# Performance work log

Measured on AMD Instinct MI355X. Metric: run time of the kernel, lower is better.

The kernel has to match this reference:

```python
import jax, jax.numpy as jnp
import numpy as np

N = 50000   # nodes
E = 800000  # edges (avg degree 16)
D = 128     # input = hidden = embedding dim
K1 = 25000  # ceil(0.5 * N)
K2 = 12500  # ceil(0.5 * K1)
LABELS = 5
BN_EPS = 1e-5


def _sage(x, src, dst, W, b, normalize):
    # old-PyG SAGEConv: remove self loops, add self loop, mean aggregate, linear, L2-normalize
    n = x.shape[0]
    dst_e = jnp.where(src == dst, n, dst)  # drop self loops; dummy edges (src=dst=n) also land in segment n
    s = jax.ops.segment_sum(x[src], dst_e, num_segments=n + 1)[:n]          # [n, d]
    deg = jax.ops.segment_sum(jnp.ones(src.shape, x.dtype), dst_e, num_segments=n + 1)[:n]
    agg = (s + x) / (deg + 1.0)[:, None]  # mean over neighbors + self
    out = agg @ W + b
    if normalize:
        out = out / jnp.maximum(jnp.linalg.norm(out, axis=-1, keepdims=True), 1e-12)
    return out


def _bn(x, g, b):
    # training-mode BatchNorm1d over nodes (biased variance, like torch)
    m = x.mean(axis=0)
    v = jnp.var(x, axis=0)
    return (x - m) / jnp.sqrt(v + BN_EPS) * g + b


def _sag_pool(x, src, dst, wp, bp, k):
    # SAGPooling: score = tanh(SAGEConv(x)->1), global top_k (single graph), filter_adj via dummy remap
    n = x.shape[0]
    score = jnp.tanh(_sage(x, src, dst, wp[:, None], bp, normalize=False)[:, 0])  # [n]
    score_k, perm = jax.lax.top_k(score, k)
    x2 = x[perm] * score_k[:, None]
    rank = jnp.full((n + 1,), -1, jnp.int32).at[perm].set(jnp.arange(k, dtype=jnp.int32))
    rs, rd = rank[src], rank[dst]
    valid = (rs >= 0) & (rd >= 0)
    src2 = jnp.where(valid, rs, k)  # invalid edges -> dummy node k
    dst2 = jnp.where(valid, rd, k)
    return x2, src2, dst2


def _forward(x, edge_index, Wc, bc, gamma, beta, Wpool, bpool, W1, b1, W2, b2):
    src, dst = edge_index[0], edge_index[1]
    # source bug replicated: stage 3 layer 2 uses bn_3_1's params
    bn_idx = [[0, 1, 2], [3, 4, 5], [6, 6, 8]]
    ks = [K1, K2]
    outs = []
    for s in range(3):
        for i in range(3):
            li = 3 * s + i
            x = jax.nn.relu(_sage(x, src, dst, Wc[li], bc[li], True))
            bi = bn_idx[s][i]
            x = _bn(x, gamma[bi], beta[bi])
        outs.append(jnp.max(x, axis=0))  # scatter_max with a single graph
        if s < 2:
            x, src, dst = _sag_pool(x, src, dst, Wpool[s], bpool[s], ks[s])
    h = jnp.concatenate(outs)[None, :]          # [1, 3*D]
    h = jax.nn.relu(h @ W1 + b1)
    return h @ W2 + b2                           # [1, LABELS]


def setup_inputs() -> dict:
    key = jax.random.key(0)
    ks = jax.random.split(key, 8)
    x = jax.random.normal(ks[0], (N, D), dtype=jnp.float32)
    edge_index = jax.random.randint(ks[1], (2, E), 0, N, dtype=jnp.int32)
    Wc = jax.random.normal(ks[2], (9, D, D), dtype=jnp.float32) / np.sqrt(D)
    bc = jnp.zeros((9, D), jnp.float32)
    gamma = jnp.ones((9, D), jnp.float32)
    beta = jnp.zeros((9, D), jnp.float32)
    Wpool = jax.random.normal(ks[3], (2, D), dtype=jnp.float32) / np.sqrt(D)
    bpool = jnp.zeros((2,), jnp.float32)
    W1 = jax.random.normal(ks[4], (3 * D, 50), dtype=jnp.float32) / np.sqrt(3 * D)
    b1 = jnp.zeros((50,), jnp.float32)
    W2 = jax.random.normal(ks[5], (50, LABELS), dtype=jnp.float32) / np.sqrt(50)
    b2 = jnp.zeros((LABELS,), jnp.float32)
    return {"x": x, "edge_index": edge_index, "Wc": Wc, "bc": bc, "gamma": gamma,
            "beta": beta, "Wpool": Wpool, "bpool": bpool,
            "W1": W1, "b1": b1, "W2": W2, "b2": b2}


def reference(x, edge_index, Wc, bc, gamma, beta, Wpool, bpool, W1, b1, W2, b2):
    return _forward(x, edge_index, Wc, bc, gamma, beta, Wpool, bpool, W1, b1, W2, b2)
```

## Files before the change

kernel.cpp:

```cpp
#include <hip/hip_runtime.h>

constexpr int FD   = 128;
constexpr int NMAX = 50000;
constexpr int EDG  = 800000;

static __device__ __forceinline__ unsigned enc(float f){
  unsigned u = __float_as_uint(f);
  return (u & 0x80000000u) ? ~u : (u | 0x80000000u);
}
static __device__ __forceinline__ float dec(unsigned e){
  unsigned u = (e & 0x80000000u) ? (e ^ 0x80000000u) : ~e;
  return __uint_as_float(u);
}

__global__ void k_count(const int* __restrict__ src, const int* __restrict__ dst,
                        int* __restrict__ deg, int E){
  int e = blockIdx.x*256 + threadIdx.x;
  if (e >= E) return;
  int s = src[e], d = dst[e];
  if (s != d) atomicAdd(&deg[d], 1);
}

__global__ void k_remap_count(const int* __restrict__ sIn, const int* __restrict__ dIn,
                              int* __restrict__ sOut, int* __restrict__ dOut,
                              const int* __restrict__ rank, int kNew,
                              int* __restrict__ deg, int E){
  int e = blockIdx.x*256 + threadIdx.x;
  if (e >= E) return;
  int s = sIn[e], d = dIn[e];
  int rs = rank[s], rd = rank[d];
  bool ok = (rs >= 0) && (rd >= 0);
  int os = ok ? rs : kNew, od = ok ? rd : kNew;
  sOut[e] = os; dOut[e] = od;
  if (os != od) atomicAdd(&deg[od], 1);
}

__global__ __launch_bounds__(256) void k_offsets(const int* __restrict__ deg,
    int* __restrict__ start, int* __restrict__ cur, int* __restrict__ total, int n){
  __shared__ int wsum[4];
  __shared__ int sbase;
  int tid = threadIdx.x, lane = tid & 63, wid = tid >> 6;
  int v = blockIdx.x*256 + tid;
  int x = (v < n) ? deg[v] : 0;
  int val = x;
  #pragma unroll
  for (int o = 1; o < 64; o <<= 1){ int t = __shfl_up(val, o); if (lane >= o) val += t; }
  if (lane == 63) wsum[wid] = val;
  __syncthreads();
  if (tid == 0){
    int t0 = wsum[0], t1 = wsum[1], t2 = wsum[2], t3 = wsum[3];
    sbase = atomicAdd(total, t0+t1+t2+t3);
    wsum[0] = 0; wsum[1] = t0; wsum[2] = t0+t1; wsum[3] = t0+t1+t2;
  }
  __syncthreads();
  int excl = (val - x) + wsum[wid] + sbase;
  if (v < n){ start[v] = excl; cur[v] = excl; }
}

__global__ void k_fill(const int* __restrict__ src, const int* __restrict__ dst,
                       int* __restrict__ cur, int* __restrict__ csr, int E){
  int e = blockIdx.x*256 + threadIdx.x;
  if (e >= E) return;
  int s = src[e], d = dst[e];
  if (s != d){ int pos = atomicAdd(&cur[d], 1); csr[pos] = s; }
}

__global__ __launch_bounds__(256) void k_agg(const float* __restrict__ X,
    const int* __restrict__ start, const int* __restrict__ degb,
    const int* __restrict__ csr,
    float* __restrict__ AGG, int n,
    const float* __restrict__ st, const float* __restrict__ g,
    const float* __restrict__ bt, float invn){
  int tid = threadIdx.x;
  int v = blockIdx.x*4 + (tid >> 6);
  if (v >= n) return;
  int lane = tid & 63;
  int c = lane * 2;
  float ax = 1.f, ay = 1.f, bx = 0.f, by = 0.f;
  if (st){
    float ma = st[c]*invn, mb = st[c+1]*invn;
    float va = st[FD+c]*invn - ma*ma, vb = st[FD+c+1]*invn - mb*mb;
    ax = g[c]*rsqrtf(va + 1e-5f);  ay = g[c+1]*rsqrtf(vb + 1e-5f);
    bx = bt[c] - ma*ax;            by = bt[c+1] - mb*ay;
  }
  int b = start[v];
  int deg = degb[v];
  float2 s = *(const float2*)(X + (size_t)v*FD + c);
  int j = 0;
  while (j < deg){
    int cnt = deg - j; if (cnt > 64) cnt = 64;
    int myu = (j + lane < deg) ? csr[b + j + lane] : 0;
    int t = 0;
    for (; t + 8 <= cnt; t += 8){
      int u0 = __shfl(myu, t),   u1 = __shfl(myu, t+1);
      int u2 = __shfl(myu, t+2), u3 = __shfl(myu, t+3);
      int u4 = __shfl(myu, t+4), u5 = __shfl(myu, t+5);
      int u6 = __shfl(myu, t+6), u7 = __shfl(myu, t+7);
      float2 t0 = *(const float2*)(X + (size_t)u0*FD + c);
      float2 t1 = *(const float2*)(X + (size_t)u1*FD + c);
      float2 t2 = *(const float2*)(X + (size_t)u2*FD + c);
      float2 t3 = *(const float2*)(X + (size_t)u3*FD + c);
      float2 t4 = *(const float2*)(X + (size_t)u4*FD + c);
      float2 t5 = *(const float2*)(X + (size_t)u5*FD + c);
      float2 t6 = *(const float2*)(X + (size_t)u6*FD + c);
      float2 t7 = *(const float2*)(X + (size_t)u7*FD + c);
      s.x += ((t0.x + t1.x) + (t2.x + t3.x)) + ((t4.x + t5.x) + (t6.x + t7.x));
      s.y += ((t0.y + t1.y) + (t2.y + t3.y)) + ((t4.y + t5.y) + (t6.y + t7.y));
    }
    for (; t + 4 <= cnt; t += 4){
      int u0 = __shfl(myu, t),   u1 = __shfl(myu, t+1);
      int u2 = __shfl(myu, t+2), u3 = __shfl(myu, t+3);
      float2 t0 = *(const float2*)(X + (size_t)u0*FD + c);
      float2 t1 = *(const float2*)(X + (size_t)u1*FD + c);
      float2 t2 = *(const float2*)(X + (size_t)u2*FD + c);
      float2 t3 = *(const float2*)(X + (size_t)u3*FD + c);
      s.x += (t0.x + t1.x) + (t2.x + t3.x);
      s.y += (t0.y + t1.y) + (t2.y + t3.y);
    }
    for (; t < cnt; t++){
      int u = __shfl(myu, t);
      float2 tt = *(const float2*)(X + (size_t)u*FD + c);
      s.x += tt.x; s.y += tt.y;
    }
    j += cnt;
  }
  float inv = 1.f / (float)(deg + 1);
  float2 o;
  o.x = s.x*inv*ax + bx;
  o.y = s.y*inv*ay + by;
  *(float2*)(AGG + (size_t)v*FD + c) = o;
}

__global__ __launch_bounds__(256,2) void k_gemm(const float* __restrict__ A,
    const float* __restrict__ W, const float* __restrict__ bias,
    float* __restrict__ Y, float* __restrict__ stats, int n,
    unsigned* __restrict__ cmx, unsigned* __restrict__ cmn){
  __shared__ float sW[FD*FD];
  __shared__ float ss[4][FD];
  __shared__ float sq_[4][FD];
  __shared__ float smx[4][FD];
  __shared__ float smn[4][FD];
  int tid = threadIdx.x;
  {
    const float4* Wg = (const float4*)W; float4* Ws = (float4*)sW;
    for (int i = tid; i < FD*FD/4; i += 256) Ws[i] = Wg[i];
  }
  __syncthreads();
  int tc = tid & 15;
  int tr = tid >> 4;
  int rbase = blockIdx.x*FD + tr*8;
  float acc[8][8];
  #pragma unroll
  for (int i = 0; i < 8; i++)
    #pragma unroll
    for (int j = 0; j < 8; j++) acc[i][j] = 0.f;

  for (int k4 = 0; k4 < FD; k4 += 4){
    float4 a[8];
    #pragma unroll
    for (int i = 0; i < 8; i++){
      int r = rbase + i; if (r >= n) r = n - 1;
      a[i] = *(const float4*)(A + (size_t)r*FD + k4);
    }
    #pragma unroll
    for (int kk = 0; kk < 4; kk++){
      const float* wr = &sW[(k4+kk)*FD + tc*8];
      float4 w0 = *(const float4*)wr, w1 = *(const float4*)(wr+4);
      #pragma unroll
      for (int i = 0; i < 8; i++){
        float av = (kk==0) ? a[i].x : (kk==1) ? a[i].y : (kk==2) ? a[i].z : a[i].w;
        acc[i][0] += av*w0.x; acc[i][1] += av*w0.y; acc[i][2] += av*w0.z; acc[i][3] += av*w0.w;
        acc[i][4] += av*w1.x; acc[i][5] += av*w1.y; acc[i][6] += av*w1.z; acc[i][7] += av*w1.w;
      }
    }
  }
  float bx[8];
  {
    const float* bp = bias + tc*8;
    #pragma unroll
    for (int j = 0; j < 8; j++) bx[j] = bp[j];
  }
  float cs[8], cq[8], mxv[8], mnv[8];
  #pragma unroll
  for (int j = 0; j < 8; j++){ cs[j]=0.f; cq[j]=0.f; mxv[j]=-3.4e38f; mnv[j]=3.4e38f; }
  #pragma unroll
  for (int i = 0; i < 8; i++){
    int r = rbase + i;
    bool valid = (r < n);
    float y[8]; float sq = 0.f;
    #pragma unroll
    for (int j = 0; j < 8; j++){ y[j] = acc[i][j] + bx[j]; sq += y[j]*y[j]; }
    sq += __shfl_xor(sq,1); sq += __shfl_xor(sq,2); sq += __shfl_xor(sq,4); sq += __shfl_xor(sq,8);
    float nrm = sqrtf(sq);
    float sc = 1.f / fmaxf(nrm, 1e-12f);
    #pragma unroll
    for (int j = 0; j < 8; j++){ y[j] *= sc; y[j] = fmaxf(y[j], 0.f); }
    if (valid){
      float* yo = Y + (size_t)r*FD + tc*8;
      *(float4*)yo     = make_float4(y[0],y[1],y[2],y[3]);
      *(float4*)(yo+4) = make_float4(y[4],y[5],y[6],y[7]);
      #pragma unroll
      for (int j = 0; j < 8; j++){
        cs[j] += y[j]; cq[j] += y[j]*y[j];
        mxv[j] = fmaxf(mxv[j], y[j]); mnv[j] = fminf(mnv[j], y[j]);
      }
    }
  }
  #pragma unroll
  for (int j = 0; j < 8; j++){
    cs[j] += __shfl_xor(cs[j],16); cs[j] += __shfl_xor(cs[j],32);
    cq[j] += __shfl_xor(cq[j],16); cq[j] += __shfl_xor(cq[j],32);
    mxv[j] = fmaxf(mxv[j], __shfl_xor(mxv[j],16)); mxv[j] = fmaxf(mxv[j], __shfl_xor(mxv[j],32));
    mnv[j] = fminf(mnv[j], __shfl_xor(mnv[j],16)); mnv[j] = fminf(mnv[j], __shfl_xor(mnv[j],32));
  }
  int wv = tid >> 6, lane = tid & 63;
  if (lane < 16){
    #pragma unroll
    for (int j = 0; j < 8; j++){
      ss[wv][tc*8+j] = cs[j]; sq_[wv][tc*8+j] = cq[j];
      smx[wv][tc*8+j] = mxv[j]; smn[wv][tc*8+j] = mnv[j];
    }
  }
  __syncthreads();
  if (tid < FD){
    float s_ = ss[0][tid]+ss[1][tid]+ss[2][tid]+ss[3][tid];
    float q_ = sq_[0][tid]+sq_[1][tid]+sq_[2][tid]+sq_[3][tid];
    atomicAdd(&stats[tid], s_);
    atomicAdd(&stats[FD+tid], q_);
    if (cmx){
      float mx = fmaxf(fmaxf(smx[0][tid],smx[1][tid]), fmaxf(smx[2][tid],smx[3][tid]));
      float mn = fminf(fminf(smn[0][tid],smn[1][tid]), fminf(smn[2][tid],smn[3][tid]));
      atomicMax(&cmx[tid], enc(mx));
      atomicMin(&cmn[tid], enc(mn));
    }
  }
}

__global__ __launch_bounds__(256) void k_dotp(const float* __restrict__ X,
    const float* __restrict__ wp,
    const float* __restrict__ st, const float* __restrict__ g,
    const float* __restrict__ bt, float invn,
    float* __restrict__ p, int n){
  int tid = threadIdx.x;
  int v = blockIdx.x*4 + (tid >> 6), lane = tid & 63;
  if (v >= n) return;
  int c = lane * 2;
  float ma = st[c]*invn, mb = st[c+1]*invn;
  float va = st[FD+c]*invn - ma*ma, vb = st[FD+c+1]*invn - mb*mb;
  float ax = g[c]*rsqrtf(va + 1e-5f), ay = g[c+1]*rsqrtf(vb + 1e-5f);
  float bx = bt[c] - ma*ax,           by = bt[c+1] - mb*ay;
  float2 x = *(const float2*)(X + (size_t)v*FD + c);
  float2 w = *(const float2*)(wp + c);
  float s = (ax*x.x + bx)*w.x + (ay*x.y + by)*w.y;
  s += __shfl_xor(s,1); s += __shfl_xor(s,2); s += __shfl_xor(s,4);
  s += __shfl_xor(s,8); s += __shfl_xor(s,16); s += __shfl_xor(s,32);
  if (lane == 0) p[v] = s;
}

__global__ void k_score(const float* __restrict__ p, const int* __restrict__ start,
    const int* __restrict__ degb, const int* __restrict__ csr,
    const float* __restrict__ bpool, int pi,
    float* __restrict__ score, unsigned* __restrict__ hist, int n){
  int v = blockIdx.x*256 + threadIdx.x;
  if (v >= n) return;
  int b = start[v], deg = degb[v];
  float s = p[v];
  for (int j = 0; j < deg; j++) s += p[csr[b+j]];
  float sc = tanhf(s / (float)(deg + 1) + bpool[pi]);
  score[v] = sc;
  atomicAdd(&hist[enc(sc) >> 16], 1u);
}

__global__ void k_hist_lo(const float* __restrict__ score, int n,
                          const unsigned* __restrict__ state, unsigned* __restrict__ hist){
  int v = blockIdx.x*256 + threadIdx.x;
  if (v >= n) return;
  unsigned key = enc(score[v]);
  if ((key >> 16) == state[5]) atomicAdd(&hist[key & 0xFFFFu], 1u);
}

__global__ __launch_bounds__(1024) void k_pick(const unsigned* __restrict__ hist,
                                               unsigned* __restrict__ state, int k, int pass){
  __shared__ unsigned wsum[16];
  int tid = threadIdx.x;
  unsigned want = (pass == 0) ? (unsigned)k : state[4];
  unsigned prevAbove = (pass == 0) ? 0u : state[1];
  int chunk = 1023 - tid;
  const unsigned* hbase = hist + chunk*64;
  unsigned csum = 0;
  #pragma unroll
  for (int j = 0; j < 64; j++) csum += hbase[j];
  unsigned val = csum;
  int lane = tid & 63, wid = tid >> 6;
  #pragma unroll
  for (int o = 1; o < 64; o <<= 1){ unsigned t = __shfl_up(val, o); if (lane >= o) val += t; }
  if (lane == 63) wsum[wid] = val;
  __syncthreads();
  if (tid < 16){
    unsigned v2 = wsum[tid];
    #pragma unroll
    for (int o = 1; o < 16; o <<= 1){ unsigned t = __shfl_up(v2, o); if (tid >= o) v2 += t; }
    wsum[tid] = v2;
  }
  __syncthreads();
  unsigned incl = val + ((wid > 0) ? wsum[wid-1] : 0u);
  unsigned excl = incl - csum;
  if (excl < want && incl >= want){
    unsigned cum = excl, above = 0; int bsel = 0;
    for (int j = 63; j >= 0; j--){
      unsigned cc = hbase[j];
      if (cum + cc >= want){ bsel = j; above = cum; break; }
      cum += cc;
    }
    unsigned bucket = (unsigned)(chunk*64 + bsel);
    if (pass == 0){
      state[5] = bucket;
      state[1] = prevAbove + above;
      state[4] = want - above;
    } else {
      unsigned T = (state[5] << 16) | bucket;
      unsigned totAbove = prevAbove + above;
      state[0] = T; state[1] = totAbove; state[2] = 0u; state[3] = totAbove;
    }
  }
}

__global__ void k_compact(const float* __restrict__ score, unsigned* __restrict__ state,
    int* __restrict__ rank, int* __restrict__ sel, int n, int k){
  int v = blockIdx.x*256 + threadIdx.x;
  if (v > n) return;
  if (v == n){ rank[n] = -1; return; }
  unsigned T = state[0];
  unsigned key = enc(score[v]);
  int slot = -1;
  if (key > T) slot = (int)atomicAdd(&state[2], 1u);
  else if (key == T){ unsigned t = atomicAdd(&state[3], 1u); if (t < (unsigned)k) slot = (int)t; }
  rank[v] = slot;
  if (slot >= 0) sel[slot] = v;
}

__global__ __launch_bounds__(256) void k_gather(const float* __restrict__ X,
    const int* __restrict__ sel, const float* __restrict__ score,
    const float* __restrict__ st, const float* __restrict__ g,
    const float* __restrict__ bt, float invn,
    float* __restrict__ XO, int k){
  int j = blockIdx.x*4 + (threadIdx.x >> 6), lane = threadIdx.x & 63;
  if (j >= k) return;
  int c = lane * 2;
  float ma = st[c]*invn, mb = st[c+1]*invn;
  float va = st[FD+c]*invn - ma*ma, vb = st[FD+c+1]*invn - mb*mb;
  float ax = g[c]*rsqrtf(va + 1e-5f), ay = g[c+1]*rsqrtf(vb + 1e-5f);
  float bx = bt[c] - ma*ax,           by = bt[c+1] - mb*ay;
  int u = sel[j];
  float sc = score[u];
  float2 t = *(const float2*)(X + (size_t)u*FD + c);
  t.x = (ax*t.x + bx)*sc; t.y = (ay*t.y + by)*sc;
  *(float2*)(XO + (size_t)j*FD + c) = t;
}

__global__ void k_final(const unsigned* __restrict__ cmx, const unsigned* __restrict__ cmn,
    const float* __restrict__ stats, const float* __restrict__ gamma,
    const float* __restrict__ beta,
    const float* __restrict__ W1, const float* __restrict__ b1,
    const float* __restrict__ W2, const float* __restrict__ b2,
    float* __restrict__ out){
  __shared__ float h[384];
  __shared__ float h1[50];
  int tid = threadIdx.x;
  if (tid < 384){
    int s = tid >> 7, c = tid & 127;
    const int liR[3] = {2,5,8};
    const float nsf[3] = {50000.f, 25000.f, 12500.f};
    int li = liR[s];
    const float* st = stats + (size_t)li*256;
    float invn = 1.f / nsf[s];
    float m = st[c]*invn, vv = st[FD+c]*invn - m*m;
    float a = gamma[(size_t)li*FD+c]*rsqrtf(vv + 1e-5f);
    float bb = beta[(size_t)li*FD+c] - m*a;
    float mx = dec(cmx[tid]), mn = dec(cmn[tid]);
    h[tid] = (a >= 0.f) ? (a*mx + bb) : (a*mn + bb);
  }
  __syncthreads();
  if (tid < 50){
    float acc = b1[tid];
    for (int i = 0; i < 384; i++) acc += h[i]*W1[i*50 + tid];
    h1[tid] = fmaxf(acc, 0.f);
  }
  __syncthreads();
  if (tid < 5){
    float acc = b2[tid];
    for (int i = 0; i < 50; i++) acc += h1[i]*W2[i*5 + tid];
    out[tid] = acc;
  }
}

extern "C" void kernel_launch(void* const* d_in, const int* in_sizes, int n_in,
                              void* d_out, int out_size, void* d_ws, size_t ws_size,
                              hipStream_t stream){
  (void)in_sizes; (void)n_in; (void)out_size; (void)ws_size;
  const float* x_in  = (const float*)d_in[0];
  const int*   ei    = (const int*)d_in[1];
  const float* Wc    = (const float*)d_in[2];
  const float* bc    = (const float*)d_in[3];
  const float* gamma = (const float*)d_in[4];
  const float* beta  = (const float*)d_in[5];
  const float* Wpool = (const float*)d_in[6];
  const float* bpool = (const float*)d_in[7];
  const float* W1    = (const float*)d_in[8];
  const float* b1    = (const float*)d_in[9];
  const float* W2    = (const float*)d_in[10];
  const float* b2    = (const float*)d_in[11];
  float* dout = (float*)d_out;

  char* base = (char*)d_ws; size_t o_ = 0;
  auto alloc = [&](size_t bytes)->void*{
    void* p = base + o_; o_ = (o_ + bytes + 255) & ~(size_t)255; return p;
  };
  float* B0   = (float*)alloc((size_t)NMAX*FD*4);
  float* B1   = (float*)alloc((size_t)NMAX*FD*4);
  int* eSrc   = (int*)alloc((size_t)EDG*4);
  int* eDst   = (int*)alloc((size_t)EDG*4);
  int* degb   = (int*)alloc((size_t)(NMAX+1)*4);
  int* startv = (int*)alloc((size_t)NMAX*4);
  int* cur    = (int*)alloc((size_t)NMAX*4);
  int* csr    = (int*)alloc((size_t)EDG*4);
  float* pbuf = (float*)alloc((size_t)NMAX*4);
  float* sbuf = (float*)alloc((size_t)NMAX*4);
  int* sel    = (int*)alloc((size_t)25000*4);
  int* rank   = (int*)alloc((size_t)(NMAX+1)*4);
  float* stats= (float*)alloc(9*256*4);
  unsigned* cmx = (unsigned*)alloc(384*4);
  unsigned* cmn = (unsigned*)alloc(384*4);
  unsigned* state= (unsigned*)alloc(64);
  unsigned* hist = (unsigned*)alloc(2*65536*4);

  const int ns[3]  = {50000, 25000, 12500};
  const int bnIdx[9] = {0,1,2,3,4,5,6,6,8};
  const int EB = (EDG + 255)/256;

  hipMemsetAsync(stats, 0, 9*256*4, stream);
  hipMemsetAsync(cmx, 0x00, 384*4, stream);
  hipMemsetAsync(cmn, 0xFF, 384*4, stream);

  const int* cs = ei;
  const int* cd = ei + EDG;

  for (int s = 0; s < 3; s++){
    int n = ns[s];
    float fin = 1.f/(float)n;
    float* X = (s == 1) ? B1 : B0;
    float* A = (s == 1) ? B0 : B1;

    hipMemsetAsync(degb, 0, (size_t)(n+1)*4, stream);
    if (s == 0){
      k_count<<<dim3(EB), dim3(256), 0, stream>>>(cs, cd, degb, EDG);
    } else {
      k_remap_count<<<dim3(EB), dim3(256), 0, stream>>>(cs, cd, eSrc, eDst, rank, n, degb, EDG);
      cs = eSrc; cd = eDst;
    }
    k_offsets<<<dim3((n+255)/256), dim3(256), 0, stream>>>(degb, startv, cur, degb + n, n);
    k_fill<<<dim3(EB), dim3(256), 0, stream>>>(cs, cd, cur, csr, EDG);

    for (int i = 0; i < 3; i++){
      int li = s*3 + i;
      const float* xr = (s == 0 && i == 0) ? x_in : (const float*)X;
      const float* stPrev = (i == 0) ? (const float*)nullptr : stats + (size_t)(li-1)*256;
      int gb = (i == 0) ? 0 : bnIdx[li-1];
      bool rd = (i == 2);
      k_agg<<<dim3((n+3)/4), dim3(256), 0, stream>>>(xr, startv, degb, csr, A, n,
                                                     stPrev, gamma + (size_t)gb*FD, beta + (size_t)gb*FD, fin);
      k_gemm<<<dim3((n+FD-1)/FD), dim3(256), 0, stream>>>(A, Wc + (size_t)li*FD*FD, bc + li*FD, X,
                                                          stats + (size_t)li*256, n,
                                                          rd ? (cmx + s*FD) : (unsigned*)nullptr,
                                                          rd ? (cmn + s*FD) : (unsigned*)nullptr);
    }

    if (s < 2){
      int k = (s == 0) ? 25000 : 12500;
      int li2 = s*3 + 2;
      const float* st2 = stats + (size_t)li2*256;
      const float* g2 = gamma + (size_t)bnIdx[li2]*FD;
      const float* bt2 = beta + (size_t)bnIdx[li2]*FD;
      hipMemsetAsync(hist, 0, 2*65536*4, stream);
      k_dotp<<<dim3((n+3)/4), dim3(256), 0, stream>>>(X, Wpool + s*FD, st2, g2, bt2, fin, pbuf, n);
      k_score<<<dim3((n+255)/256), dim3(256), 0, stream>>>(pbuf, startv, degb, csr, bpool, s, sbuf, hist, n);
      k_pick<<<1, 1024, 0, stream>>>(hist, state, k, 0);
      k_hist_lo<<<dim3((n+255)/256), dim3(256), 0, stream>>>(sbuf, n, state, hist + 65536);
      k_pick<<<1, 1024, 0, stream>>>(hist + 65536, state, k, 1);
      k_compact<<<dim3((n+256)/256), dim3(256), 0, stream>>>(sbuf, state, rank, sel, n, k);
      k_gather<<<dim3((k+3)/4), dim3(256), 0, stream>>>(X, sel, sbuf, st2, g2, bt2, fin, A, k);
    }
  }
  k_final<<<1, 384, 0, stream>>>(cmx, cmn, stats, gamma, beta, W1, b1, W2, b2, dout);
}
```

Before: 962.3 us.

## Store node features in bf16 for neighbor aggregation and parallelize score kernel

Node features read by the gather-heavy aggregation kernel are now stored as bf16 copies written by the GEMM epilogue, the input conversion kernel, and the pooling gather. This halves the bytes moved by the random neighbor reads. The fp32 output is kept only where pooling needs it. The score kernel now uses one wavefront per node instead of one thread per node, and the histogram memset is folded into the dot-product kernel. The cost is bf16 rounding in the aggregated features, which may change the top-k selection.

Result: faster. 928.7 us (-3.5%).

```diff
diff --git a/kernel.cpp b/kernel.cpp
--- a/kernel.cpp
+++ b/kernel.cpp
@@ -11,6 +11,23 @@
 static __device__ __forceinline__ float dec(unsigned e){
   unsigned u = (e & 0x80000000u) ? (e ^ 0x80000000u) : ~e;
   return __uint_as_float(u);
+}
+static __device__ __forceinline__ unsigned short f2bf(float f){
+  unsigned u = __float_as_uint(f);
+  unsigned r = u + 0x7FFFu + ((u >> 16) & 1u);
+  return (unsigned short)(r >> 16);
+}
+static __device__ __forceinline__ float bf2f(unsigned short h){
+  return __uint_as_float(((unsigned)h) << 16);
+}
+
+__global__ __launch_bounds__(256) void k_cvt(const float* __restrict__ in,
+                                             unsigned short* __restrict__ out, int n2){
+  int i = blockIdx.x*256 + threadIdx.x;
+  if (i >= n2) return;
+  float2 v = ((const float2*)in)[i];
+  ushort2 o; o.x = f2bf(v.x); o.y = f2bf(v.y);
+  ((ushort2*)out)[i] = o;
 }
 
 __global__ void k_count(const int* __restrict__ src, const int* __restrict__ dst,
@@ -65,7 +82,7 @@
   if (s != d){ int pos = atomicAdd(&cur[d], 1); csr[pos] = s; }
 }
 
-__global__ __launch_bounds__(256) void k_agg(const float* __restrict__ X,
+__global__ __launch_bounds__(256) void k_agg(const unsigned short* __restrict__ Xbf,
     const int* __restrict__ start, const int* __restrict__ degb,
     const int* __restrict__ csr,
     float* __restrict__ AGG, int n,
@@ -85,7 +102,8 @@
   }
   int b = start[v];
   int deg = degb[v];
-  float2 s = *(const float2*)(X + (size_t)v*FD + c);
+  ushort2 sv = *(const ushort2*)(Xbf + (size_t)v*FD + c);
+  float sx = bf2f(sv.x), sy = bf2f(sv.y);
   int j = 0;
   while (j < deg){
     int cnt = deg - j; if (cnt > 64) cnt = 64;
@@ -96,44 +114,37 @@
       int u2 = __shfl(myu, t+2), u3 = __shfl(myu, t+3);
       int u4 = __shfl(myu, t+4), u5 = __shfl(myu, t+5);
       int u6 = __shfl(myu, t+6), u7 = __shfl(myu, t+7);
-      float2 t0 = *(const float2*)(X + (size_t)u0*FD + c);
-      float2 t1 = *(const float2*)(X + (size_t)u1*FD + c);
-      float2 t2 = *(const float2*)(X + (size_t)u2*FD + c);
-      float2 t3 = *(const float2*)(X + (size_t)u3*FD + c);
-      float2 t4 = *(const float2*)(X + (size_t)u4*FD + c);
-      float2 t5 = *(const float2*)(X + (size_t)u5*FD + c);
-      float2 t6 = *(const float2*)(X + (size_t)u6*FD + c);
-      float2 t7 = *(const float2*)(X + (size_t)u7*FD + c);
-      s.x += ((t0.x + t1.x) + (t2.x + t3.x)) + ((t4.x + t5.x) + (t6.x + t7.x));
-      s.y += ((t0.y + t1.y) + (t2.y + t3.y)) + ((t4.y + t5.y) + (t6.y + t7.y));
-    }
-    for (; t + 4 <= cnt; t += 4){
-      int u0 = __shfl(myu, t),   u1 = __shfl(myu, t+1);
-      int u2 = __shfl(myu, t+2), u3 = __shfl(myu, t+3);
-      float2 t0 = *(const float2*)(X + (size_t)u0*FD + c);
-      float2 t1 = *(const float2*)(X + (size_t)u1*FD + c);
-      float2 t2 = *(const float2*)(X + (size_t)u2*FD + c);
-      float2 t3 = *(const float2*)(X + (size_t)u3*FD + c);
-      s.x += (t0.x + t1.x) + (t2.x + t3.x);
-      s.y += (t0.y + t1.y) + (t2.y + t3.y);
+      ushort2 t0 = *(const ushort2*)(Xbf + (size_t)u0*FD + c);
+      ushort2 t1 = *(const ushort2*)(Xbf + (size_t)u1*FD + c);
+      ushort2 t2 = *(const ushort2*)(Xbf + (size_t)u2*FD + c);
+      ushort2 t3 = *(const ushort2*)(Xbf + (size_t)u3*FD + c);
+      ushort2 t4 = *(const ushort2*)(Xbf + (size_t)u4*FD + c);
+      ushort2 t5 = *(const ushort2*)(Xbf + (size_t)u5*FD + c);
+      ushort2 t6 = *(const ushort2*)(Xbf + (size_t)u6*FD + c);
+      ushort2 t7 = *(const ushort2*)(Xbf + (size_t)u7*FD + c);
+      sx += ((bf2f(t0.x)+bf2f(t1.x)) + (bf2f(t2.x)+bf2f(t3.x)))
+          + ((bf2f(t4.x)+bf2f(t5.x)) + (bf2f(t6.x)+bf2f(t7.x)));
+      sy += ((bf2f(t0.y)+bf2f(t1.y)) + (bf2f(t2.y)+bf2f(t3.y)))
+          + ((bf2f(t4.y)+bf2f(t5.y)) + (bf2f(t6.y)+bf2f(t7.y)));
     }
     for (; t < cnt; t++){
       int u = __shfl(myu, t);
-      float2 tt = *(const float2*)(X + (size_t)u*FD + c);
-      s.x += tt.x; s.y += tt.y;
+      ushort2 tt = *(const ushort2*)(Xbf + (size_t)u*FD + c);
+      sx += bf2f(tt.x); sy += bf2f(tt.y);
     }
     j += cnt;
   }
   float inv = 1.f / (float)(deg + 1);
   float2 o;
-  o.x = s.x*inv*ax + bx;
-  o.y = s.y*inv*ay + by;
+  o.x = sx*inv*ax + bx;
+  o.y = sy*inv*ay + by;
   *(float2*)(AGG + (size_t)v*FD + c) = o;
 }
 
 __global__ __launch_bounds__(256,2) void k_gemm(const float* __restrict__ A,
     const float* __restrict__ W, const float* __restrict__ bias,
-    float* __restrict__ Y, float* __restrict__ stats, int n,
+    float* __restrict__ Y, unsigned short* __restrict__ Ybf,
+    float* __restrict__ stats, int n,
     unsigned* __restrict__ cmx, unsigned* __restrict__ cmn){
   __shared__ float sW[FD*FD];
   __shared__ float ss[4][FD];
@@ -196,9 +207,16 @@
     #pragma unroll
     for (int j = 0; j < 8; j++){ y[j] *= sc; y[j] = fmaxf(y[j], 0.f); }
     if (valid){
-      float* yo = Y + (size_t)r*FD + tc*8;
-      *(float4*)yo     = make_float4(y[0],y[1],y[2],y[3]);
-      *(float4*)(yo+4) = make_float4(y[4],y[5],y[6],y[7]);
+      if (Y){
+        float* yo = Y + (size_t)r*FD + tc*8;
+        *(float4*)yo     = make_float4(y[0],y[1],y[2],y[3]);
+        *(float4*)(yo+4) = make_float4(y[4],y[5],y[6],y[7]);
+      }
+      unsigned pk0 = (unsigned)f2bf(y[0]) | ((unsigned)f2bf(y[1])<<16);
+      unsigned pk1 = (unsigned)f2bf(y[2]) | ((unsigned)f2bf(y[3])<<16);
+      unsigned pk2 = (unsigned)f2bf(y[4]) | ((unsigned)f2bf(y[5])<<16);
+      unsigned pk3 = (unsigned)f2bf(y[6]) | ((unsigned)f2bf(y[7])<<16);
+      *(uint4*)(Ybf + (size_t)r*FD + tc*8) = make_uint4(pk0,pk1,pk2,pk3);
       #pragma unroll
       for (int j = 0; j < 8; j++){
         cs[j] += y[j]; cq[j] += y[j]*y[j];
@@ -240,8 +258,9 @@
     const float* __restrict__ wp,
     const float* __restrict__ st, const float* __restrict__ g,
     const float* __restrict__ bt, float invn,
-    float* __restrict__ p, int n){
+    float* __restrict__ p, unsigned* __restrict__ hist, int n){
   int tid = threadIdx.x;
+  if (blockIdx.x < 512) hist[blockIdx.x*256 + tid] = 0u;
   int v = blockIdx.x*4 + (tid >> 6), lane = tid & 63;
   if (v >= n) return;
   int c = lane * 2;
@@ -257,18 +276,24 @@
   if (lane == 0) p[v] = s;
 }
 
-__global__ void k_score(const float* __restrict__ p, const int* __restrict__ start,
-    const int* __restrict__ degb, const int* __restrict__ csr,
-    const float* __restrict__ bpool, int pi,
+__global__ __launch_bounds__(256) void k_score(const float* __restrict__ p,
+    const int* __restrict__ start, const int* __restrict__ degb,
+    const int* __restrict__ csr, const float* __restrict__ bpool, int pi,
     float* __restrict__ score, unsigned* __restrict__ hist, int n){
-  int v = blockIdx.x*256 + threadIdx.x;
+  int tid = threadIdx.x, lane = tid & 63;
+  int v = blockIdx.x*4 + (tid >> 6);
   if (v >= n) return;
   int b = start[v], deg = degb[v];
-  float s = p[v];
-  for (int j = 0; j < deg; j++) s += p[csr[b+j]];
-  float sc = tanhf(s / (float)(deg + 1) + bpool[pi]);
-  score[v] = sc;
-  atomicAdd(&hist[enc(sc) >> 16], 1u);
+  float s = 0.f;
+  for (int j = lane; j < deg; j += 64) s += p[csr[b+j]];
+  s += __shfl_xor(s,1); s += __shfl_xor(s,2); s += __shfl_xor(s,4);
+  s += __shfl_xor(s,8); s += __shfl_xor(s,16); s += __shfl_xor(s,32);
+  if (lane == 0){
+    s += p[v];
+    float sc = tanhf(s / (float)(deg + 1) + bpool[pi]);
+    score[v] = sc;
+    atomicAdd(&hist[enc(sc) >> 16], 1u);
+  }
 }
 
 __global__ void k_hist_lo(const float* __restrict__ score, int n,
@@ -343,7 +368,7 @@
     const int* __restrict__ sel, const float* __restrict__ score,
     const float* __restrict__ st, const float* __restrict__ g,
     const float* __restrict__ bt, float invn,
-    float* __restrict__ XO, int k){
+    unsigned short* __restrict__ XObf, int k){
   int j = blockIdx.x*4 + (threadIdx.x >> 6), lane = threadIdx.x & 63;
   if (j >= k) return;
   int c = lane * 2;
@@ -354,8 +379,10 @@
   int u = sel[j];
   float sc = score[u];
   float2 t = *(const float2*)(X + (size_t)u*FD + c);
-  t.x = (ax*t.x + bx)*sc; t.y = (ay*t.y + by)*sc;
-  *(float2*)(XO + (size_t)j*FD + c) = t;
+  ushort2 o;
+  o.x = f2bf((ax*t.x + bx)*sc);
+  o.y = f2bf((ay*t.y + by)*sc);
+  *(ushort2*)(XObf + (size_t)j*FD + c) = o;
 }
 
 __global__ void k_final(const unsigned* __restrict__ cmx, const unsigned* __restrict__ cmn,
@@ -418,6 +445,8 @@
   };
   float* B0   = (float*)alloc((size_t)NMAX*FD*4);
   float* B1   = (float*)alloc((size_t)NMAX*FD*4);
+  unsigned short* B0bf = (unsigned short*)alloc((size_t)NMAX*FD*2);
+  unsigned short* B1bf = (unsigned short*)alloc((size_t)NMAX*FD*2);
   int* eSrc   = (int*)alloc((size_t)EDG*4);
   int* eDst   = (int*)alloc((size_t)EDG*4);
   int* degb   = (int*)alloc((size_t)(NMAX+1)*4);
@@ -442,6 +471,8 @@
   hipMemsetAsync(cmx, 0x00, 384*4, stream);
   hipMemsetAsync(cmn, 0xFF, 384*4, stream);
 
+  k_cvt<<<dim3((NMAX*FD/2 + 255)/256), dim3(256), 0, stream>>>(x_in, B0bf, NMAX*FD/2);
+
   const int* cs = ei;
   const int* cd = ei + EDG;
 
@@ -449,7 +480,9 @@
     int n = ns[s];
     float fin = 1.f/(float)n;
     float* X = (s == 1) ? B1 : B0;
+    unsigned short* Xbf = (s == 1) ? B1bf : B0bf;
     float* A = (s == 1) ? B0 : B1;
+    unsigned short* Abf = (s == 1) ? B0bf : B1bf;
 
     hipMemsetAsync(degb, 0, (size_t)(n+1)*4, stream);
     if (s == 0){
@@ -463,13 +496,14 @@
 
     for (int i = 0; i < 3; i++){
       int li = s*3 + i;
-      const float* xr = (s == 0 && i == 0) ? x_in : (const float*)X;
       const float* stPrev = (i == 0) ? (const float*)nullptr : stats + (size_t)(li-1)*256;
       int gb = (i == 0) ? 0 : bnIdx[li-1];
       bool rd = (i == 2);
-      k_agg<<<dim3((n+3)/4), dim3(256), 0, stream>>>(xr, startv, degb, csr, A, n,
+      bool writeF = (i == 2) && (s < 2);
+      k_agg<<<dim3((n+3)/4), dim3(256), 0, stream>>>(Xbf, startv, degb, csr, A, n,
                                                      stPrev, gamma + (size_t)gb*FD, beta + (size_t)gb*FD, fin);
-      k_gemm<<<dim3((n+FD-1)/FD), dim3(256), 0, stream>>>(A, Wc + (size_t)li*FD*FD, bc + li*FD, X,
+      k_gemm<<<dim3((n+FD-1)/FD), dim3(256), 0, stream>>>(A, Wc + (size_t)li*FD*FD, bc + li*FD,
+                                                          writeF ? X : (float*)nullptr, Xbf,
                                                           stats + (size_t)li*256, n,
                                                           rd ? (cmx + s*FD) : (unsigned*)nullptr,
                                                           rd ? (cmn + s*FD) : (unsigned*)nullptr);
@@ -481,14 +515,13 @@
       const float* st2 = stats + (size_t)li2*256;
       const float* g2 = gamma + (size_t)bnIdx[li2]*FD;
       const float* bt2 = beta + (size_t)bnIdx[li2]*FD;
-      hipMemsetAsync(hist, 0, 2*65536*4, stream);
-      k_dotp<<<dim3((n+3)/4), dim3(256), 0, stream>>>(X, Wpool + s*FD, st2, g2, bt2, fin, pbuf, n);
-      k_score<<<dim3((n+255)/256), dim3(256), 0, stream>>>(pbuf, startv, degb, csr, bpool, s, sbuf, hist, n);
+      k_dotp<<<dim3((n+3)/4), dim3(256), 0, stream>>>(X, Wpool + s*FD, st2, g2, bt2, fin, pbuf, hist, n);
+      k_score<<<dim3((n+3)/4), dim3(256), 0, stream>>>(pbuf, startv, degb, csr, bpool, s, sbuf, hist, n);
       k_pick<<<1, 1024, 0, stream>>>(hist, state, k, 0);
       k_hist_lo<<<dim3((n+255)/256), dim3(256), 0, stream>>>(sbuf, n, state, hist + 65536);
       k_pick<<<1, 1024, 0, stream>>>(hist + 65536, state, k, 1);
       k_compact<<<dim3((n+256)/256), dim3(256), 0, stream>>>(sbuf, state, rank, sel, n, k);
-      k_gather<<<dim3((k+3)/4), dim3(256), 0, stream>>>(X, sel, sbuf, st2, g2, bt2, fin, A, k);
+      k_gather<<<dim3((k+3)/4), dim3(256), 0, stream>>>(X, sel, sbuf, st2, g2, bt2, fin, Abf, k);
     }
   }
   k_final<<<1, 384, 0, stream>>>(cmx, cmn, stats, gamma, beta, W1, b1, W2, b2, dout);
```
